# Kernel optimization log

Hardware: AMD Instinct MI355X
Metric: run time of the kernel (lower is better)

## Reference

```python
import jax, jax.numpy as jnp
import numpy as np

N_NODES = 50000
W_IN = 256
W_OUT = 256
HEADS = 8
D_HEAD = W_OUT // HEADS
NUM_EDGE = 3
N_EDGES = 800000
NEG_SLOPE = 0.2


def setup_inputs() -> dict:
    key = jax.random.key(0)
    ks = jax.random.split(key, 10)
    x = jax.random.normal(ks[0], (N_NODES, W_IN), dtype=jnp.float32)
    adj = jax.random.randint(ks[1], (NUM_EDGE, 2, N_EDGES), 0, N_NODES, dtype=jnp.int64)
    sw = 1.0 / np.sqrt(W_IN)
    # Per-edge-type GATConv params, stacked on leading edge-type axis
    Ws = jax.random.normal(ks[2], (NUM_EDGE, W_IN, HEADS * D_HEAD), dtype=jnp.float32) * sw
    a_l = jax.random.normal(ks[3], (NUM_EDGE, HEADS, D_HEAD), dtype=jnp.float32) * 0.1
    a_r = jax.random.normal(ks[4], (NUM_EDGE, HEADS, D_HEAD), dtype=jnp.float32) * 0.1
    bias = jnp.zeros((NUM_EDGE, HEADS * D_HEAD), dtype=jnp.float32)
    # Semantic attention layer: Linear(w_out -> 1)
    att_w = jax.random.normal(ks[5], (W_OUT, 1), dtype=jnp.float32) * (1.0 / np.sqrt(W_OUT))
    att_b = jnp.zeros((1,), dtype=jnp.float32)
    return {"x": x, "adj": adj, "Ws": Ws, "a_l": a_l, "a_r": a_r,
            "bias": bias, "att_w": att_w, "att_b": att_b}


def _gat(x, edge_index, W, al, ar, b):
    # x: [N, W_IN]; edge_index: [2, E]; W: [W_IN, H*D]; al/ar: [H, D]; b: [H*D]
    N = x.shape[0]
    h = (x @ W).reshape(N, HEADS, D_HEAD)            # [N, H, D]
    src, dst = edge_index[0], edge_index[1]
    el = jnp.einsum('nhd,hd->nh', h, al)             # src-side scores [N, H]
    er = jnp.einsum('nhd,hd->nh', h, ar)             # dst-side scores [N, H]
    e = jax.nn.leaky_relu(el[src] + er[dst], NEG_SLOPE)   # [E, H]
    # segment softmax over incoming edges of each dst node
    m = jax.ops.segment_max(e, dst, num_segments=N)       # [N, H]
    e = jnp.exp(e - m[dst])
    s = jax.ops.segment_sum(e, dst, num_segments=N)       # [N, H]
    alpha = e / (s[dst] + 1e-9)                           # [E, H]
    out = jax.ops.segment_sum(alpha[:, :, None] * h[src], dst, num_segments=N)
    return out.reshape(N, HEADS * D_HEAD) + b             # concat heads [N, W_OUT]


def reference(x, adj, Ws, a_l, a_r, bias, att_w, att_b):
    outs = [_gat(x, adj[i], Ws[i], a_l[i], a_r[i], bias[i]) for i in range(NUM_EDGE)]
    stacked = jnp.stack(outs, axis=1)                     # [N, T, W_OUT]
    # AttentionLayer: scores = Linear(stacked) viewed as [N, 1, T]; NO softmax (faithful)
    att = (stacked @ att_w + att_b).reshape(-1, 1, NUM_EDGE)  # [N, 1, T]
    return jnp.matmul(att, stacked).squeeze(1)            # [N, W_OUT]
```

## Files before the change

### kernel.cpp

```cpp
#include <hip/hip_runtime.h>

#define N_NODES 50000
#define W_IN    256
#define W_OUT   256
#define HEADS   8
#define NUM_T   3
#define N_EDGES 800000
#define NEG_SLOPE 0.2f

#define NB      128
#define BSH     9
#define BNODES  512
#define P1_EPT  16
#define P1_CHUNK (256 * P1_EPT)
#define P1_BLOCKS ((N_EDGES + P1_CHUNK - 1) / P1_CHUNK)
#define NB_USED ((N_NODES + BNODES - 1) / BNODES)

#define GEMM_BLOCKS ((N_NODES + 63) / 64)
#define GATHER_BLOCKS ((N_NODES + 3) / 4)
#define GEMM_SMEM 25600

typedef __attribute__((ext_vector_type(8))) short bf16x8;
typedef __attribute__((ext_vector_type(4))) float f32x4;

__device__ __forceinline__ unsigned short f2b(float f) {
    unsigned u = __float_as_uint(f);
    u = (u + 0x7fffu + ((u >> 16) & 1u)) >> 16;
    return (unsigned short)u;
}
__device__ __forceinline__ float blo(unsigned u) { return __uint_as_float(u << 16); }
__device__ __forceinline__ float bhi(unsigned u) { return __uint_as_float(u & 0xffff0000u); }

__global__ __launch_bounds__(256) void convert_x(const float* __restrict__ x,
                                                 unsigned short* __restrict__ xb) {
    const size_t i = ((size_t)blockIdx.x * 256 + threadIdx.x) * 4;
    const float4 v = *(const float4*)(x + i);
    ushort4 o;
    o.x = f2b(v.x); o.y = f2b(v.y); o.z = f2b(v.z); o.w = f2b(v.w);
    *(ushort4*)(xb + i) = o;
}

__global__ __launch_bounds__(256) void convert_W(const float* __restrict__ Wsrc,
                                                 unsigned short* __restrict__ Wt) {
    const int t = blockIdx.y;
    const int gid = blockIdx.x * 256 + threadIdx.x;
    const int k = gid >> 8, n = gid & 255;
    Wt[(size_t)t * 65536 + (size_t)n * 256 + k] = f2b(Wsrc[(size_t)t * 65536 + gid]);
}

__global__ __launch_bounds__(256) void p1_hist(const int* __restrict__ adj,
                                               int* __restrict__ bucket_cnt) {
    __shared__ int lh[NB];
    const int t = blockIdx.y;
    const int tid = threadIdx.x;
    if (tid < NB) lh[tid] = 0;
    __syncthreads();

    const int* dstp = adj + (size_t)t * 2 * N_EDGES + N_EDGES;
    const int e0 = blockIdx.x * P1_CHUNK + tid * P1_EPT;
#pragma unroll
    for (int i = 0; i < P1_EPT; ++i) {
        const int e = e0 + i;
        if (e < N_EDGES) atomicAdd(&lh[dstp[e] >> BSH], 1);
    }
    __syncthreads();
    if (tid < NB && lh[tid] > 0) atomicAdd(&bucket_cnt[t * NB + tid], lh[tid]);
}

__global__ __launch_bounds__(128) void p1_scan(const int* __restrict__ bucket_cnt,
                                               int* __restrict__ bucket_ptr,
                                               int* __restrict__ bucket_cur) {
    __shared__ int s[NB];
    const int tid = threadIdx.x;
    for (int t = 0; t < NUM_T; ++t) {
        const int v = bucket_cnt[t * NB + tid];
        s[tid] = v;
        __syncthreads();
        for (int off = 1; off < NB; off <<= 1) {
            int o = (tid >= off) ? s[tid - off] : 0;
            __syncthreads();
            s[tid] += o;
            __syncthreads();
        }
        const int incl = s[tid];
        const int excl = incl - v;
        bucket_ptr[t * (NB + 1) + tid] = excl;
        bucket_cur[t * NB + tid] = excl;
        if (tid == NB - 1) bucket_ptr[t * (NB + 1) + NB] = incl;
        __syncthreads();
    }
}

__global__ __launch_bounds__(256) void p1_scatter(const int* __restrict__ adj,
                                                  int* __restrict__ bucket_cur,
                                                  uint2* __restrict__ part) {
    __shared__ int lh[NB];
    __shared__ int loff[NB];
    __shared__ int lbase[NB];
    __shared__ uint2 buf[P1_CHUNK];
    const int t = blockIdx.y;
    const int tid = threadIdx.x;
    const int lane = tid & 63;
    const int wave = tid >> 6;
    if (tid < NB) lh[tid] = 0;
    __syncthreads();

    const int* srcp = adj + (size_t)t * 2 * N_EDGES;
    const int* dstp = srcp + N_EDGES;
    const int e0 = blockIdx.x * P1_CHUNK + tid * P1_EPT;

    int es[P1_EPT], ed[P1_EPT], rk[P1_EPT];
#pragma unroll
    for (int i = 0; i < P1_EPT; ++i) {
        const int e = e0 + i;
        if (e < N_EDGES) {
            es[i] = srcp[e];
            ed[i] = dstp[e];
            rk[i] = atomicAdd(&lh[ed[i] >> BSH], 1);
        } else {
            ed[i] = -1;
        }
    }
    __syncthreads();

    if (tid < NB && lh[tid] > 0)
        lbase[tid] = atomicAdd(&bucket_cur[t * NB + tid], lh[tid]);
    if (wave == 0) {
        const int c0 = lh[lane * 2], c1 = lh[lane * 2 + 1];
        const int s = c0 + c1;
        int run = s;
        for (int off = 1; off < 64; off <<= 1) {
            const int o = __shfl_up(run, off);
            if (lane >= off) run += o;
        }
        const int base = run - s;
        loff[lane * 2] = base;
        loff[lane * 2 + 1] = base + c0;
    }
    __syncthreads();

#pragma unroll
    for (int i = 0; i < P1_EPT; ++i)
        if (ed[i] >= 0)
            buf[loff[ed[i] >> BSH] + rk[i]] =
                make_uint2((unsigned)es[i], (unsigned)ed[i]);
    __syncthreads();

    uint2* pt = part + (size_t)t * N_EDGES;
    int nvalid = N_EDGES - blockIdx.x * P1_CHUNK;
    if (nvalid > P1_CHUNK) nvalid = P1_CHUNK;
    for (int idx = tid; idx < nvalid; idx += 256) {
        const uint2 e = buf[idx];
        const int b = (int)(e.y >> BSH);
        pt[lbase[b] + (idx - loff[b])] = e;
    }
}

__global__ __launch_bounds__(256) void p2_csr(const uint2* __restrict__ part,
                                              const int* __restrict__ bucket_ptr,
                                              int* __restrict__ row_ptr_all,
                                              int* __restrict__ csr_all) {
    __shared__ int sc[BNODES];
    const int b = blockIdx.x;
    const int t = blockIdx.y;
    const int tid = threadIdx.x;
    const int lane = tid & 63;
    const int wave = tid >> 6;

    const uint2* pt = part + (size_t)t * N_EDGES;
    int* row_ptr = row_ptr_all + (size_t)t * (N_NODES + 1);
    int* csr = csr_all + (size_t)t * N_EDGES;

    const int bp0 = bucket_ptr[t * (NB + 1) + b];
    const int bp1 = bucket_ptr[t * (NB + 1) + b + 1];
    const int node0 = b * BNODES;
    int nn = N_NODES - node0; if (nn > BNODES) nn = BNODES;

    sc[tid] = 0; sc[tid + 256] = 0;
    __syncthreads();

    for (int idx = bp0 + tid; idx < bp1; idx += 256)
        atomicAdd(&sc[pt[idx].y - node0], 1);
    __syncthreads();

    if (wave == 0) {
        int v[8], ex[8];
        int s = 0;
#pragma unroll
        for (int i = 0; i < 8; ++i) { v[i] = sc[lane * 8 + i]; ex[i] = s; s += v[i]; }
        int run = s;
        for (int off = 1; off < 64; off <<= 1) {
            int o = __shfl_up(run, off);
            if (lane >= off) run += o;
        }
        const int base = run - s;
#pragma unroll
        for (int i = 0; i < 8; ++i) sc[lane * 8 + i] = base + ex[i];
    }
    __syncthreads();

    for (int i = tid; i < nn; i += 256) row_ptr[node0 + i] = bp0 + sc[i];
    if (b == NB_USED - 1 && tid == 0) row_ptr[N_NODES] = N_EDGES;
    __syncthreads();

    for (int idx = bp0 + tid; idx < bp1; idx += 256) {
        const uint2 e = pt[idx];
        const int pos = bp0 + atomicAdd(&sc[e.y - node0], 1);
        csr[pos] = (int)e.x;
    }
}

__device__ __forceinline__ void gemm_body(const int bm, const int tid,
                                          unsigned char* smem,
                                          const unsigned short* __restrict__ xb,
                                          const unsigned short* __restrict__ Wt,
                                          unsigned short* __restrict__ H) {
    unsigned short* As = (unsigned short*)smem;
    unsigned short* Bs = (unsigned short*)(smem + 5120);

    const int wave = tid >> 6;
    const int lane = tid & 63;
    const int quad = lane >> 4;
    const int l16 = lane & 15;
    const int m0 = bm * 64;

    f32x4 acc[4][4] = {};

    const int arow = tid >> 2;
    const int achunk = (tid & 3) * 8;
    int gm = m0 + arow;
    if (gm > N_NODES - 1) gm = N_NODES - 1;
    const unsigned short* aptr = xb + (size_t)gm * W_IN + achunk;

    for (int k0 = 0; k0 < W_IN; k0 += 32) {
        const uint4 av = *(const uint4*)(aptr + k0);
        *(uint4*)&As[arow * 40 + achunk] = av;
#pragma unroll
        for (int i = 0; i < 4; ++i) {
            const int idx = i * 256 + tid;
            const int brow = idx >> 2;
            const int bch = (idx & 3) * 8;
            const uint4 bv = *(const uint4*)(Wt + (size_t)brow * W_IN + k0 + bch);
            *(uint4*)&Bs[brow * 40 + bch] = bv;
        }
        __syncthreads();

        bf16x8 af[4], bfr[4];
#pragma unroll
        for (int mi = 0; mi < 4; ++mi)
            af[mi] = *(const bf16x8*)&As[(mi * 16 + l16) * 40 + quad * 8];
#pragma unroll
        for (int ni = 0; ni < 4; ++ni)
            bfr[ni] = *(const bf16x8*)&Bs[(wave * 64 + ni * 16 + l16) * 40 + quad * 8];
#pragma unroll
        for (int mi = 0; mi < 4; ++mi)
#pragma unroll
            for (int ni = 0; ni < 4; ++ni)
                acc[mi][ni] = __builtin_amdgcn_mfma_f32_16x16x32_bf16(
                    af[mi], bfr[ni], acc[mi][ni], 0, 0, 0);
        __syncthreads();
    }

#pragma unroll
    for (int mi = 0; mi < 4; ++mi)
#pragma unroll
        for (int reg = 0; reg < 4; ++reg) {
            const int gr = m0 + mi * 16 + quad * 4 + reg;
            if (gr < N_NODES)
#pragma unroll
                for (int ni = 0; ni < 4; ++ni)
                    H[(size_t)gr * W_OUT + wave * 64 + ni * 16 + l16] =
                        f2b(acc[mi][ni][reg]);
        }
}

__global__ __launch_bounds__(256) void gemm_fused(const unsigned short* __restrict__ xb,
                                                  const unsigned short* __restrict__ Wt,
                                                  unsigned short* __restrict__ H) {
    __shared__ __attribute__((aligned(16))) unsigned char smem[GEMM_SMEM];
    const size_t t = blockIdx.y;
    gemm_body(blockIdx.x, threadIdx.x, smem, xb,
              Wt + t * 65536,
              H + t * (size_t)N_NODES * W_OUT);
}

__global__ __launch_bounds__(256) void compute_elr(
    const unsigned short* __restrict__ H, const float* __restrict__ a_l,
    const float* __restrict__ a_r, float* __restrict__ el,
    float* __restrict__ er) {
    const int node = (blockIdx.x * blockDim.x + threadIdx.x) >> 6;
    if (node >= N_NODES) return;
    const int t = blockIdx.y;
    const int lane = threadIdx.x & 63;
    const int h = lane >> 3;
    const int j8 = lane & 7;

    const size_t row = (size_t)t * N_NODES + node;
    const uint2 u = *(const uint2*)(H + row * W_OUT + h * 32 + j8 * 4);
    const float4 av = *(const float4*)(a_l + t * 256 + h * 32 + j8 * 4);
    const float4 rv = *(const float4*)(a_r + t * 256 + h * 32 + j8 * 4);
    const float c0 = blo(u.x), c1 = bhi(u.x), c2 = blo(u.y), c3 = bhi(u.y);
    float pl = c0 * av.x + c1 * av.y + c2 * av.z + c3 * av.w;
    float pr = c0 * rv.x + c1 * rv.y + c2 * rv.z + c3 * rv.w;
#pragma unroll
    for (int off = 1; off < 8; off <<= 1) {
        pl += __shfl_xor(pl, off);
        pr += __shfl_xor(pr, off);
    }
    if (j8 == 0) el[row * HEADS + h] = pl;
    if (j8 == 1) er[row * HEADS + h] = pr;
}

__device__ __forceinline__ void gather_accum(const int node, const int lane,
                                             const int* __restrict__ csr_src,
                                             const int* __restrict__ row_ptr,
                                             const float* __restrict__ el,
                                             const float* __restrict__ er,
                                             const unsigned short* __restrict__ H,
                                             float2 (&acc)[4], float& ssum) {
    const int half = lane >> 5;
    const int d8 = lane & 31;
    const int hh = d8 >> 2;

    const int beg = row_ptr[node];
    const int deg = row_ptr[node + 1] - beg;
    if (deg <= 0) return;
    const float erv = er[(size_t)node * HEADS + hh];

    int mysrc = (lane < deg) ? csr_src[beg + lane] : 0;
    const int npairs = (deg + 1) >> 1;

    int src0 = __shfl(mysrc, half);
    uint4 u0 = *(const uint4*)(H + (size_t)src0 * W_OUT + d8 * 8);
    float elv0 = el[(size_t)src0 * HEADS + hh];

    for (int q = 0; q < npairs; ++q) {
        int src1 = 0; uint4 u1 = u0; float elv1 = 0.f;
        const int q1 = q + 1;
        if (q1 < npairs) {
            if ((q1 & 31) == 0) {
                const int cb = beg + (q1 >> 5) * 64;
                mysrc = (cb + lane < beg + deg) ? csr_src[cb + lane] : 0;
            }
            src1 = __shfl(mysrc, (2 * q1 + half) & 63);
            u1 = *(const uint4*)(H + (size_t)src1 * W_OUT + d8 * 8);
            elv1 = el[(size_t)src1 * HEADS + hh];
        }
        float v = elv0 + erv;
        v = (v > 0.f) ? v : NEG_SLOPE * v;
        const float w = (2 * q + half < deg) ? __expf(v) : 0.f;
        acc[0].x += w * blo(u0.x); acc[0].y += w * bhi(u0.x);
        acc[1].x += w * blo(u0.y); acc[1].y += w * bhi(u0.y);
        acc[2].x += w * blo(u0.z); acc[2].y += w * bhi(u0.z);
        acc[3].x += w * blo(u0.w); acc[3].y += w * bhi(u0.w);
        ssum += w;
        src0 = src1; u0 = u1; elv0 = elv1;
    }
}

__global__ __launch_bounds__(256) void gat_gather_all(
    const int* __restrict__ csr_src, const int* __restrict__ row_ptr,
    const float* __restrict__ el, const float* __restrict__ er,
    const unsigned short* __restrict__ H,
    const float* __restrict__ bias, const float* __restrict__ att_w,
    const float* __restrict__ att_b, float* __restrict__ out) {
    const int node = (blockIdx.x * blockDim.x + threadIdx.x) >> 6;
    const int lane = threadIdx.x & 63;
    if (node >= N_NODES) return;

    float2 acc[NUM_T][4] = {};
    float ssum[NUM_T] = {};

#pragma unroll
    for (int t = 0; t < NUM_T; ++t)
        gather_accum(node, lane,
                     csr_src + (size_t)t * N_EDGES,
                     row_ptr + (size_t)t * (N_NODES + 1),
                     el + (size_t)t * N_NODES * HEADS,
                     er + (size_t)t * N_NODES * HEADS,
                     H + (size_t)t * N_NODES * W_OUT,
                     acc[t], ssum[t]);

#pragma unroll
    for (int t = 0; t < NUM_T; ++t) {
#pragma unroll
        for (int i = 0; i < 4; ++i) {
            acc[t][i].x += __shfl_xor(acc[t][i].x, 32);
            acc[t][i].y += __shfl_xor(acc[t][i].y, 32);
        }
        ssum[t] += __shfl_xor(ssum[t], 32);
    }

    const int half = lane >> 5;
    const int d8 = lane & 31;
    if (half == 0) {
        const float4 aw0 = *(const float4*)(att_w + d8 * 8);
        const float4 aw1 = *(const float4*)(att_w + d8 * 8 + 4);
        float h[NUM_T][8];
        float p[NUM_T];
#pragma unroll
        for (int t = 0; t < NUM_T; ++t) {
            const float inv = 1.f / (ssum[t] + 1e-9f);
            const float4 b0 = *(const float4*)(bias + t * W_OUT + d8 * 8);
            const float4 b1 = *(const float4*)(bias + t * W_OUT + d8 * 8 + 4);
            h[t][0] = acc[t][0].x * inv + b0.x;
            h[t][1] = acc[t][0].y * inv + b0.y;
            h[t][2] = acc[t][1].x * inv + b0.z;
            h[t][3] = acc[t][1].y * inv + b0.w;
            h[t][4] = acc[t][2].x * inv + b1.x;
            h[t][5] = acc[t][2].y * inv + b1.y;
            h[t][6] = acc[t][3].x * inv + b1.z;
            h[t][7] = acc[t][3].y * inv + b1.w;
            p[t] = h[t][0] * aw0.x + h[t][1] * aw0.y + h[t][2] * aw0.z +
                   h[t][3] * aw0.w + h[t][4] * aw1.x + h[t][5] * aw1.y +
                   h[t][6] * aw1.z + h[t][7] * aw1.w;
        }
#pragma unroll
        for (int off = 1; off < 32; off <<= 1) {
            p[0] += __shfl_xor(p[0], off);
            p[1] += __shfl_xor(p[1], off);
            p[2] += __shfl_xor(p[2], off);
        }
        const float ab = att_b[0];
        const float a0 = p[0] + ab, a1 = p[1] + ab, a2 = p[2] + ab;
        float4 o0, o1;
        o0.x = a0 * h[0][0] + a1 * h[1][0] + a2 * h[2][0];
        o0.y = a0 * h[0][1] + a1 * h[1][1] + a2 * h[2][1];
        o0.z = a0 * h[0][2] + a1 * h[1][2] + a2 * h[2][2];
        o0.w = a0 * h[0][3] + a1 * h[1][3] + a2 * h[2][3];
        o1.x = a0 * h[0][4] + a1 * h[1][4] + a2 * h[2][4];
        o1.y = a0 * h[0][5] + a1 * h[1][5] + a2 * h[2][5];
        o1.z = a0 * h[0][6] + a1 * h[1][6] + a2 * h[2][6];
        o1.w = a0 * h[0][7] + a1 * h[1][7] + a2 * h[2][7];
        *(float4*)(out + (size_t)node * W_OUT + d8 * 8) = o0;
        *(float4*)(out + (size_t)node * W_OUT + d8 * 8 + 4) = o1;
    }
}

extern "C" void kernel_launch(void* const* d_in, const int* in_sizes, int n_in,
                              void* d_out, int out_size, void* d_ws, size_t ws_size,
                              hipStream_t stream) {
    const float* x     = (const float*)d_in[0];
    const int*   adj   = (const int*)d_in[1];
    const float* Ws    = (const float*)d_in[2];
    const float* a_l   = (const float*)d_in[3];
    const float* a_r   = (const float*)d_in[4];
    const float* bias  = (const float*)d_in[5];
    const float* att_w = (const float*)d_in[6];
    const float* att_b = (const float*)d_in[7];
    float* out = (float*)d_out;

    char* w = (char*)d_ws;
    unsigned short* xb = (unsigned short*)w; w += (size_t)N_NODES * W_IN * 2;
    unsigned short* H  = (unsigned short*)w; w += (size_t)NUM_T * N_NODES * W_OUT * 2;
    unsigned short* Wt = (unsigned short*)w; w += (size_t)NUM_T * 65536 * 2;
    float* el = (float*)w; w += (size_t)NUM_T * N_NODES * HEADS * 4;
    float* er = (float*)w; w += (size_t)NUM_T * N_NODES * HEADS * 4;
    int* csr_src = (int*)w; w += (size_t)NUM_T * N_EDGES * 4;
    int* row_ptr = (int*)w; w += (size_t)NUM_T * (N_NODES + 1) * 4;
    int* bucket_cnt = (int*)w; w += NUM_T * NB * 4;
    int* bucket_ptr = (int*)w; w += NUM_T * (NB + 1) * 4;
    int* bucket_cur = (int*)w; w += NUM_T * NB * 4;
    uint2* part = (uint2*)H;

    hipMemsetAsync(bucket_cnt, 0, NUM_T * NB * sizeof(int), stream);
    convert_x<<<12500, 256, 0, stream>>>(x, xb);
    convert_W<<<dim3(256, NUM_T), 256, 0, stream>>>(Ws, Wt);
    p1_hist<<<dim3(P1_BLOCKS, NUM_T), 256, 0, stream>>>(adj, bucket_cnt);
    p1_scan<<<1, 128, 0, stream>>>(bucket_cnt, bucket_ptr, bucket_cur);
    p1_scatter<<<dim3(P1_BLOCKS, NUM_T), 256, 0, stream>>>(adj, bucket_cur, part);
    p2_csr<<<dim3(NB_USED, NUM_T), 256, 0, stream>>>(part, bucket_ptr, row_ptr,
                                                     csr_src);

    gemm_fused<<<dim3(GEMM_BLOCKS, NUM_T), 256, 0, stream>>>(xb, Wt, H);

    compute_elr<<<dim3(GATHER_BLOCKS, NUM_T), 256, 0, stream>>>(H, a_l, a_r,
                                                                el, er);

    gat_gather_all<<<GATHER_BLOCKS, 256, 0, stream>>>(
        csr_src, row_ptr, el, er, H, bias, att_w, att_b, out);
}
```

Before: 467.2 us.

## Retile GEMM to 128x128 blocks with direct global-to-LDS loads

Changes the projection GEMM from 64x256 tiles to 128x128 tiles over a 3D grid, with each wave computing a 64x64 subtile. When the global_load_lds builtin is available, A and B tiles are loaded straight from global memory into LDS instead of going through registers. The LDS row padding (stride 40) is dropped for an unpadded stride of 32, which may add bank conflicts on the fragment reads. The intent is more balanced reuse per tile and less register traffic for staging, at the cost of reading A twice across the N split.

```diff
diff --git a/kernel.cpp b/kernel.cpp
--- a/kernel.cpp
+++ b/kernel.cpp
@@ -16,9 +16,14 @@
 #define P1_BLOCKS ((N_EDGES + P1_CHUNK - 1) / P1_CHUNK)
 #define NB_USED ((N_NODES + BNODES - 1) / BNODES)
 
-#define GEMM_BLOCKS ((N_NODES + 63) / 64)
+#define MT_BLOCKS ((N_NODES + 127) / 128)
 #define GATHER_BLOCKS ((N_NODES + 3) / 4)
-#define GEMM_SMEM 25600
+
+#if defined(__has_builtin)
+#if __has_builtin(__builtin_amdgcn_global_load_lds)
+#define HAS_GLL 1
+#endif
+#endif
 
 typedef __attribute__((ext_vector_type(8))) short bf16x8;
 typedef __attribute__((ext_vector_type(4))) float f32x4;
@@ -210,48 +215,78 @@
     }
 }
 
-__device__ __forceinline__ void gemm_body(const int bm, const int tid,
-                                          unsigned char* smem,
-                                          const unsigned short* __restrict__ xb,
-                                          const unsigned short* __restrict__ Wt,
-                                          unsigned short* __restrict__ H) {
-    unsigned short* As = (unsigned short*)smem;
-    unsigned short* Bs = (unsigned short*)(smem + 5120);
-
+__global__ __launch_bounds__(256) void gemm_fused(const unsigned short* __restrict__ xb,
+                                                  const unsigned short* __restrict__ Wt,
+                                                  unsigned short* __restrict__ H) {
+    __shared__ __attribute__((aligned(16))) unsigned short As[128 * 32];
+    __shared__ __attribute__((aligned(16))) unsigned short Bs[128 * 32];
+
+    const int tid  = threadIdx.x;
     const int wave = tid >> 6;
     const int lane = tid & 63;
     const int quad = lane >> 4;
-    const int l16 = lane & 15;
-    const int m0 = bm * 64;
+    const int l16  = lane & 15;
+
+    const int m0 = blockIdx.x * 128;
+    const int n0 = blockIdx.y * 128;
+    const int t  = blockIdx.z;
+
+    const unsigned short* Bt = Wt + (size_t)t * 65536 + (size_t)n0 * W_IN;
+    unsigned short* Hc = H + (size_t)t * N_NODES * W_OUT;
+
+    const int moff = (wave >> 1) * 64;
+    const int noff = (wave & 1) * 64;
 
     f32x4 acc[4][4] = {};
 
-    const int arow = tid >> 2;
-    const int achunk = (tid & 3) * 8;
-    int gm = m0 + arow;
-    if (gm > N_NODES - 1) gm = N_NODES - 1;
-    const unsigned short* aptr = xb + (size_t)gm * W_IN + achunk;
+    const int srow = tid >> 2;
+    const int sch  = (tid & 3) * 8;
+    int ar0 = m0 + srow;       if (ar0 > N_NODES - 1) ar0 = N_NODES - 1;
+    int ar1 = m0 + 64 + srow;  if (ar1 > N_NODES - 1) ar1 = N_NODES - 1;
+    const unsigned short* a0p = xb + (size_t)ar0 * W_IN + sch;
+    const unsigned short* a1p = xb + (size_t)ar1 * W_IN + sch;
+    const unsigned short* b0p = Bt + (size_t)srow * W_IN + sch;
+    const unsigned short* b1p = Bt + (size_t)(64 + srow) * W_IN + sch;
+#if defined(HAS_GLL)
+    const int ldso0 = wave * 64 * 8;
+    const int ldso1 = (256 + wave * 64) * 8;
+#endif
 
     for (int k0 = 0; k0 < W_IN; k0 += 32) {
-        const uint4 av = *(const uint4*)(aptr + k0);
-        *(uint4*)&As[arow * 40 + achunk] = av;
-#pragma unroll
-        for (int i = 0; i < 4; ++i) {
-            const int idx = i * 256 + tid;
-            const int brow = idx >> 2;
-            const int bch = (idx & 3) * 8;
-            const uint4 bv = *(const uint4*)(Wt + (size_t)brow * W_IN + k0 + bch);
-            *(uint4*)&Bs[brow * 40 + bch] = bv;
-        }
+#if defined(HAS_GLL)
+        __builtin_amdgcn_global_load_lds(
+            (const __attribute__((address_space(1))) void*)(a0p + k0),
+            (__attribute__((address_space(3))) void*)(As + ldso0), 16, 0, 0);
+        __builtin_amdgcn_global_load_lds(
+            (const __attribute__((address_space(1))) void*)(a1p + k0),
+            (__attribute__((address_space(3))) void*)(As + ldso1), 16, 0, 0);
+        __builtin_amdgcn_global_load_lds(
+            (const __attribute__((address_space(1))) void*)(b0p + k0),
+            (__attribute__((address_space(3))) void*)(Bs + ldso0), 16, 0, 0);
+        __builtin_amdgcn_global_load_lds(
+            (const __attribute__((address_space(1))) void*)(b1p + k0),
+            (__attribute__((address_space(3))) void*)(Bs + ldso1), 16, 0, 0);
+#else
+        {
+            const uint4 av0 = *(const uint4*)(a0p + k0);
+            const uint4 av1 = *(const uint4*)(a1p + k0);
+            const uint4 bv0 = *(const uint4*)(b0p + k0);
+            const uint4 bv1 = *(const uint4*)(b1p + k0);
+            *(uint4*)&As[(size_t)tid * 8] = av0;
+            *(uint4*)&As[2048 + (size_t)tid * 8] = av1;
+            *(uint4*)&Bs[(size_t)tid * 8] = bv0;
+            *(uint4*)&Bs[2048 + (size_t)tid * 8] = bv1;
+        }
+#endif
         __syncthreads();
 
         bf16x8 af[4], bfr[4];
 #pragma unroll
         for (int mi = 0; mi < 4; ++mi)
-            af[mi] = *(const bf16x8*)&As[(mi * 16 + l16) * 40 + quad * 8];
+            af[mi] = *(const bf16x8*)&As[(moff + mi * 16 + l16) * 32 + quad * 8];
 #pragma unroll
         for (int ni = 0; ni < 4; ++ni)
-            bfr[ni] = *(const bf16x8*)&Bs[(wave * 64 + ni * 16 + l16) * 40 + quad * 8];
+            bfr[ni] = *(const bf16x8*)&Bs[(noff + ni * 16 + l16) * 32 + quad * 8];
 #pragma unroll
         for (int mi = 0; mi < 4; ++mi)
 #pragma unroll
@@ -265,23 +300,13 @@
     for (int mi = 0; mi < 4; ++mi)
 #pragma unroll
         for (int reg = 0; reg < 4; ++reg) {
-            const int gr = m0 + mi * 16 + quad * 4 + reg;
+            const int gr = m0 + moff + mi * 16 + quad * 4 + reg;
             if (gr < N_NODES)
 #pragma unroll
                 for (int ni = 0; ni < 4; ++ni)
-                    H[(size_t)gr * W_OUT + wave * 64 + ni * 16 + l16] =
+                    Hc[(size_t)gr * W_OUT + n0 + noff + ni * 16 + l16] =
                         f2b(acc[mi][ni][reg]);
         }
-}
-
-__global__ __launch_bounds__(256) void gemm_fused(const unsigned short* __restrict__ xb,
-                                                  const unsigned short* __restrict__ Wt,
-                                                  unsigned short* __restrict__ H) {
-    __shared__ __attribute__((aligned(16))) unsigned char smem[GEMM_SMEM];
-    const size_t t = blockIdx.y;
-    gemm_body(blockIdx.x, threadIdx.x, smem, xb,
-              Wt + t * 65536,
-              H + t * (size_t)N_NODES * W_OUT);
 }
 
 __global__ __launch_bounds__(256) void compute_elr(
@@ -472,7 +497,7 @@
     p2_csr<<<dim3(NB_USED, NUM_T), 256, 0, stream>>>(part, bucket_ptr, row_ptr,
                                                      csr_src);
 
-    gemm_fused<<<dim3(GEMM_BLOCKS, NUM_T), 256, 0, stream>>>(xb, Wt, H);
+    gemm_fused<<<dim3(MT_BLOCKS, 2, NUM_T), 256, 0, stream>>>(xb, Wt, H);
 
     compute_elr<<<dim3(GATHER_BLOCKS, NUM_T), 256, 0, stream>>>(H, a_l, a_r,
                                                                 el, er);
```

New measurement: 462.8 us. No clear change (-0.9%).
